# Optimization experiments

Hardware: AMD Instinct MI355X
Metric: run time of the kernel (lower is better)

Reference implementation:

```python
import jax, jax.numpy as jnp
import numpy as np

M, K, V, A = 50, 50, 200, 64  # memory_size, key_dim, value_dim, attention_dim
B, S = 512, 1024


def setup_inputs() -> dict:
    key = jax.random.key(0)
    ks = jax.random.split(key, 12)
    kaiming = lambda k, shape, fan_in: jax.random.normal(k, shape, jnp.float32) * np.sqrt(2.0 / fan_in)
    return {
        "query_embeddings": jax.random.normal(ks[0], (B, S, K), jnp.float32),
        "attention_features": jax.random.normal(ks[1], (B, S, A), jnp.float32),
        "value_memory": jax.random.normal(ks[2], (B, M, V), jnp.float32),
        "key_memory": kaiming(ks[3], (M, K), K),
        "Wc": kaiming(ks[4], (K, K), K),   # correlation_projection
        "bc": jnp.zeros((K,), jnp.float32),
        "Wr": kaiming(ks[5], (A, V), V),   # guided_read_projection
        "br": jnp.zeros((A,), jnp.float32),
        "We": kaiming(ks[6], (V, 2 * A), 2 * A),  # erase_gate
        "be": jnp.zeros((V,), jnp.float32),
        "Wa": kaiming(ks[7], (V, 2 * A), 2 * A),  # add_gate
        "ba": jnp.zeros((V,), jnp.float32),
    }


def reference(query_embeddings, attention_features, value_memory,
              key_memory, Wc, bc, Wr, br, We, be, Wa, ba):
    # update_memory=True path: sequential DKVMN read/erase/add over time.

    def read(mem, q_t, a_t):
        ck = jnp.tanh(q_t @ Wc.T + bc)                     # [B,K]
        w = jax.nn.softmax(ck @ key_memory.T, axis=-1)     # [B,M]
        rc = jnp.einsum('bm,bmv->bv', w, mem) @ Wr.T + br  # [B,A]
        return w, rc

    def write(mem, w, a_t, rc):
        wi = jnp.concatenate([a_t, rc], axis=-1)           # [B,2A]
        erase = jax.nn.sigmoid(wi @ We.T + be)             # [B,V]
        add = jnp.tanh(wi @ Wa.T + ba)                     # [B,V]
        w3 = w[:, :, None]
        return mem * (1.0 - w3 * erase[:, None, :]) + w3 * add[:, None, :]

    def step(mem, xs):
        q_t, a_t = xs
        w, rc = read(mem, q_t, a_t)
        return write(mem, w, a_t, rc), (rc, w)

    # first S-1 steps update memory; last step reads only
    q_seq = jnp.swapaxes(query_embeddings[:, :-1], 0, 1)   # [S-1,B,K]
    a_seq = jnp.swapaxes(attention_features[:, :-1], 0, 1)
    mem_final, (rcs, ws) = jax.lax.scan(step, value_memory, (q_seq, a_seq))
    w_last, rc_last = read(mem_final, query_embeddings[:, -1], attention_features[:, -1])

    read_content = jnp.concatenate([jnp.swapaxes(rcs, 0, 1), rc_last[:, None]], axis=1)  # [B,S,A]
    memory_weights = jnp.concatenate([jnp.swapaxes(ws, 0, 1), w_last[:, None]], axis=1)  # [B,S,M]
    return read_content, mem_final, memory_weights
```

## Files before the change

### kernel.cpp

```cpp
#include <hip/hip_runtime.h>
#include <stdint.h>

#define Md 50
#define Kd 50
#define Vd 200
#define Ad 64
#define Bd 512
#define Sd 1024

__device__ __forceinline__ float fast_tanh(float x) {
    float e = __expf(2.f * x);
    return 1.f - 2.f / (e + 1.f);
}

__device__ __forceinline__ float sigmoidf_(float x) {
    return 1.f / (1.f + __expf(-x));
}

__global__ __launch_bounds__(256)
void wpre_kernel(const float* __restrict__ q_in,
                 const float* __restrict__ key_in,
                 const float* __restrict__ Wc_in,
                 const float* __restrict__ bc_in,
                 float* __restrict__ w_out)
{
    __shared__ float sWc[Kd * 51];
    __shared__ float sKey[Md * 51];
    __shared__ float sbc[Kd];
    __shared__ __align__(16) float sbuf[4][64];

    const int tid = threadIdx.x;
    for (int idx = tid; idx < Kd * Kd; idx += 256) {
        int i = idx / Kd, j = idx % Kd;
        sWc[i * 51 + j]  = Wc_in[idx];
        sKey[i * 51 + j] = key_in[idx];
    }
    if (tid < Kd) sbc[tid] = bc_in[tid];
    __syncthreads();

    const int wv = tid >> 6, ln = tid & 63;
    const int gw = blockIdx.x * 4 + wv;

    for (int r = 0; r < 64; ++r) {
        const size_t row = (size_t)gw * 64 + r;
        float qv = 0.f;
        if (ln < Kd) qv = q_in[row * Kd + ln];
        sbuf[wv][ln] = qv;
        __syncthreads();

        float ck = 0.f;
        if (ln < Kd) {
            const float4* qp = (const float4*)sbuf[wv];
            float acc = sbc[ln];
            #pragma unroll
            for (int c = 0; c < 12; ++c) {
                float4 x = qp[c];
                acc = fmaf(x.x, sWc[ln * 51 + 4 * c + 0], acc);
                acc = fmaf(x.y, sWc[ln * 51 + 4 * c + 1], acc);
                acc = fmaf(x.z, sWc[ln * 51 + 4 * c + 2], acc);
                acc = fmaf(x.w, sWc[ln * 51 + 4 * c + 3], acc);
            }
            float2 x2 = *(const float2*)&sbuf[wv][48];
            acc = fmaf(x2.x, sWc[ln * 51 + 48], acc);
            acc = fmaf(x2.y, sWc[ln * 51 + 49], acc);
            ck = fast_tanh(acc);
        }
        __syncthreads();
        sbuf[wv][ln] = ck;
        __syncthreads();

        float lg = -1e30f;
        if (ln < Md) {
            const float4* cp = (const float4*)sbuf[wv];
            float acc = 0.f;
            #pragma unroll
            for (int c = 0; c < 12; ++c) {
                float4 x = cp[c];
                acc = fmaf(x.x, sKey[ln * 51 + 4 * c + 0], acc);
                acc = fmaf(x.y, sKey[ln * 51 + 4 * c + 1], acc);
                acc = fmaf(x.z, sKey[ln * 51 + 4 * c + 2], acc);
                acc = fmaf(x.w, sKey[ln * 51 + 4 * c + 3], acc);
            }
            float2 x2 = *(const float2*)&sbuf[wv][48];
            acc = fmaf(x2.x, sKey[ln * 51 + 48], acc);
            acc = fmaf(x2.y, sKey[ln * 51 + 49], acc);
            lg = acc;
        }
        float mx = lg;
        #pragma unroll
        for (int off = 32; off > 0; off >>= 1)
            mx = fmaxf(mx, __shfl_xor(mx, off));
        float e = (ln < Md) ? __expf(lg - mx) : 0.f;
        float sm = e;
        #pragma unroll
        for (int off = 32; off > 0; off >>= 1)
            sm += __shfl_xor(sm, off);
        if (ln < Md) w_out[row * Md + ln] = e / sm;
        __syncthreads();
    }
}

__global__ __launch_bounds__(512, 2)
void agm_kernel(const float* __restrict__ a_in,
                const float* __restrict__ mem_in,
                const float* __restrict__ Wr_in,
                const float* __restrict__ br_in,
                const float* __restrict__ We_in,
                const float* __restrict__ be_in,
                const float* __restrict__ Wa_in,
                const float* __restrict__ ba_in,
                const float* __restrict__ w_in,
                float* __restrict__ rc_out,
                float* __restrict__ mem_out)
{
    __shared__ float sWrT[Vd * 66];
    __shared__ float sbr[Ad];
    __shared__ __align__(16) float swi[2][128];
    __shared__ __align__(16) float sw[2][2][64];
    __shared__ float spe[2][2][Vd];
    __shared__ float spa[2][2][Vd];
    __shared__ __align__(8) float srcvI[Vd * 2];

    const int tid = threadIdx.x;
    const int blk = blockIdx.x;
    const int hb  = tid >> 8;
    const int mv  = tid & 255;
    const int bidx = blk * 2 + hb;

    for (int idx = tid; idx < Ad * Vd; idx += 512) {
        int a = idx / Vd, v = idx % Vd;
        sWrT[v * 66 + a] = Wr_in[idx];
    }
    if (tid < Ad) sbr[tid] = br_in[tid];

    const bool isW = (tid < 400);
    const int r5  = tid % 200;
    const int wh5 = tid / 200;
    float WeC[64], WaC[64];
    if (isW) {
        const float4* wep = (const float4*)(We_in + (size_t)r5 * 128 + wh5 * 64);
        const float4* wap = (const float4*)(Wa_in + (size_t)r5 * 128 + wh5 * 64);
        #pragma unroll
        for (int c = 0; c < 16; ++c) {
            float4 ue = wep[c], ua = wap[c];
            WeC[4*c+0]=ue.x; WeC[4*c+1]=ue.y; WeC[4*c+2]=ue.z; WeC[4*c+3]=ue.w;
            WaC[4*c+0]=ua.x; WaC[4*c+1]=ua.y; WaC[4*c+2]=ua.z; WaC[4*c+3]=ua.w;
        }
    } else {
        #pragma unroll
        for (int j = 0; j < 64; ++j) { WeC[j] = 0.f; WaC[j] = 0.f; }
    }

    const bool isM = (mv < Vd);
    float memcol[Md];
    float ebias = 0.f, abias = 0.f;
    if (isM) {
        #pragma unroll
        for (int m = 0; m < Md; ++m)
            memcol[m] = mem_in[(size_t)bidx * Md * Vd + m * Vd + mv];
        ebias = be_in[mv];
        abias = ba_in[mv];
    } else {
        #pragma unroll
        for (int m = 0; m < Md; ++m) memcol[m] = 0.f;
    }

    const int g4 = (tid >> 3) & 31;
    const int c4 = tid & 7;

    const bool isA = (tid < 128);
    const int ahb = tid >> 6, aj = tid & 63;
    const bool isWw = (tid >= 128 && tid < 228);
    const int whb = (tid - 128) / 50, wm = (tid - 128) % 50;

    auto s4_phase = [&](int tt) {
        float q00 = 0.f, q01 = 0.f, q10 = 0.f, q11 = 0.f;
        #pragma unroll
        for (int j = 0; j < 25; ++j) {
            int v = c4 * 25 + j;
            float2 sv = *(const float2*)&srcvI[v * 2];
            float2 wr = *(const float2*)&sWrT[v * 66 + 2 * g4];
            q00 = fmaf(sv.x, wr.x, q00);
            q01 = fmaf(sv.y, wr.x, q01);
            q10 = fmaf(sv.x, wr.y, q10);
            q11 = fmaf(sv.y, wr.y, q11);
        }
        #pragma unroll
        for (int off = 1; off < 8; off <<= 1) {
            q00 += __shfl_xor(q00, off);
            q01 += __shfl_xor(q01, off);
            q10 += __shfl_xor(q10, off);
            q11 += __shfl_xor(q11, off);
        }
        if (c4 == 0) {
            int a0 = 2 * g4, a1 = a0 + 1;
            float rc00 = q00 + sbr[a0], rc01 = q01 + sbr[a0];
            float rc10 = q10 + sbr[a1], rc11 = q11 + sbr[a1];
            swi[0][64 + a0] = rc00; swi[1][64 + a0] = rc01;
            swi[0][64 + a1] = rc10; swi[1][64 + a1] = rc11;
            size_t o0 = ((size_t)(blk * 2 + 0) * Sd + tt) * Ad;
            size_t o1 = ((size_t)(blk * 2 + 1) * Sd + tt) * Ad;
            rc_out[o0 + a0] = rc00; rc_out[o1 + a0] = rc01;
            rc_out[o0 + a1] = rc10; rc_out[o1 + a1] = rc11;
        }
    };

    if (tid < 100) {
        int b = tid / 50, m = tid % 50;
        sw[0][b][m] = w_in[((size_t)(blk * 2 + b) * Sd + 0) * Md + m];
        sw[1][b][m] = w_in[((size_t)(blk * 2 + b) * Sd + 1) * Md + m];
    }
    if (isA) swi[ahb][aj] = a_in[((size_t)(blk * 2 + ahb) * Sd + 0) * Ad + aj];
    float areg = 0.f, wreg = 0.f;
    if (isA) areg = a_in[((size_t)(blk * 2 + ahb) * Sd + 1) * Ad + aj];
    if (isWw) wreg = w_in[((size_t)(blk * 2 + whb) * Sd + 2) * Md + wm];
    __syncthreads();

    if (isM) {
        const float4* w0p = (const float4*)sw[0][hb];
        float rv0 = 0.f, rv1 = 0.f;
        #pragma unroll
        for (int c = 0; c < 12; ++c) {
            float4 wa = w0p[c];
            rv0 = fmaf(wa.x, memcol[4*c+0], rv0);
            rv1 = fmaf(wa.y, memcol[4*c+1], rv1);
            rv0 = fmaf(wa.z, memcol[4*c+2], rv0);
            rv1 = fmaf(wa.w, memcol[4*c+3], rv1);
        }
        float2 wa2 = *(const float2*)&sw[0][hb][48];
        rv0 = fmaf(wa2.x, memcol[48], rv0);
        rv1 = fmaf(wa2.y, memcol[49], rv1);
        srcvI[mv * 2 + hb] = rv0 + rv1;
    }
    __syncthreads();
    if (tid >= 256) s4_phase(0);
    __syncthreads();

    for (int t = 0; t < Sd - 1; ++t) {
        if (isW) {
            const float4* x0p = (const float4*)&swi[0][wh5 * 64];
            const float4* x1p = (const float4*)&swi[1][wh5 * 64];
            float pe0 = 0.f, pa0 = 0.f, pe1 = 0.f, pa1 = 0.f;
            #pragma unroll
            for (int c = 0; c < 16; ++c) {
                float4 x0 = x0p[c];
                float4 x1 = x1p[c];
                float w0 = WeC[4*c+0], w1 = WeC[4*c+1], w2 = WeC[4*c+2], w3 = WeC[4*c+3];
                float u0 = WaC[4*c+0], u1 = WaC[4*c+1], u2 = WaC[4*c+2], u3 = WaC[4*c+3];
                pe0 = fmaf(x0.x, w0, pe0); pe0 = fmaf(x0.y, w1, pe0);
                pe0 = fmaf(x0.z, w2, pe0); pe0 = fmaf(x0.w, w3, pe0);
                pa0 = fmaf(x0.x, u0, pa0); pa0 = fmaf(x0.y, u1, pa0);
                pa0 = fmaf(x0.z, u2, pa0); pa0 = fmaf(x0.w, u3, pa0);
                pe1 = fmaf(x1.x, w0, pe1); pe1 = fmaf(x1.y, w1, pe1);
                pe1 = fmaf(x1.z, w2, pe1); pe1 = fmaf(x1.w, w3, pe1);
                pa1 = fmaf(x1.x, u0, pa1); pa1 = fmaf(x1.y, u1, pa1);
                pa1 = fmaf(x1.z, u2, pa1); pa1 = fmaf(x1.w, u3, pa1);
            }
            spe[wh5][0][r5] = pe0; spe[wh5][1][r5] = pe1;
            spa[wh5][0][r5] = pa0; spa[wh5][1][r5] = pa1;
        }
        __syncthreads();

        if (isM) {
            float se_ = spe[0][hb][mv] + spe[1][hb][mv] + ebias;
            float sa_ = spa[0][hb][mv] + spa[1][hb][mv] + abias;
            float ev = sigmoidf_(se_);
            float av = fast_tanh(sa_);
            const float4* w0p = (const float4*)sw[t & 1][hb];
            const float4* w1p = (const float4*)sw[(t + 1) & 1][hb];
            float rv0 = 0.f, rv1 = 0.f;
            #pragma unroll
            for (int c = 0; c < 12; ++c) {
                float4 wa = w0p[c];
                float4 wb = w1p[c];
                { float mc = memcol[4*c+0]; mc = fmaf(wa.x, fmaf(-ev, mc, av), mc);
                  memcol[4*c+0] = mc; rv0 = fmaf(wb.x, mc, rv0); }
                { float mc = memcol[4*c+1]; mc = fmaf(wa.y, fmaf(-ev, mc, av), mc);
                  memcol[4*c+1] = mc; rv1 = fmaf(wb.y, mc, rv1); }
                { float mc = memcol[4*c+2]; mc = fmaf(wa.z, fmaf(-ev, mc, av), mc);
                  memcol[4*c+2] = mc; rv0 = fmaf(wb.z, mc, rv0); }
                { float mc = memcol[4*c+3]; mc = fmaf(wa.w, fmaf(-ev, mc, av), mc);
                  memcol[4*c+3] = mc; rv1 = fmaf(wb.w, mc, rv1); }
            }
            {
                float2 wa2 = *(const float2*)&sw[t & 1][hb][48];
                float2 wb2 = *(const float2*)&sw[(t + 1) & 1][hb][48];
                { float mc = memcol[48]; mc = fmaf(wa2.x, fmaf(-ev, mc, av), mc);
                  memcol[48] = mc; rv0 = fmaf(wb2.x, mc, rv0); }
                { float mc = memcol[49]; mc = fmaf(wa2.y, fmaf(-ev, mc, av), mc);
                  memcol[49] = mc; rv1 = fmaf(wb2.y, mc, rv1); }
            }
            srcvI[mv * 2 + hb] = rv0 + rv1;
        }
        __syncthreads();

        if (tid >= 256) {
            s4_phase(t + 1);
        } else {
            if (isA) swi[ahb][aj] = areg;
            if (isWw && t + 2 < Sd) sw[t & 1][whb][wm] = wreg;
        }
        if (isA && t + 2 < Sd)
            areg = a_in[((size_t)(blk * 2 + ahb) * Sd + (t + 2)) * Ad + aj];
        if (isWw && t + 3 < Sd)
            wreg = w_in[((size_t)(blk * 2 + whb) * Sd + (t + 3)) * Md + wm];
        __syncthreads();
    }

    if (isM) {
        #pragma unroll
        for (int m = 0; m < Md; ++m)
            mem_out[(size_t)bidx * Md * Vd + m * Vd + mv] = memcol[m];
    }
}

extern "C" void kernel_launch(void* const* d_in, const int* in_sizes, int n_in,
                              void* d_out, int out_size, void* d_ws, size_t ws_size,
                              hipStream_t stream) {
    const float* q   = (const float*)d_in[0];
    const float* a   = (const float*)d_in[1];
    const float* mem = (const float*)d_in[2];
    const float* key = (const float*)d_in[3];
    const float* Wc  = (const float*)d_in[4];
    const float* bc  = (const float*)d_in[5];
    const float* Wr  = (const float*)d_in[6];
    const float* br  = (const float*)d_in[7];
    const float* We  = (const float*)d_in[8];
    const float* be  = (const float*)d_in[9];
    const float* Wa  = (const float*)d_in[10];
    const float* ba  = (const float*)d_in[11];

    float* out = (float*)d_out;
    float* rc_out  = out;
    float* mem_out = rc_out + (size_t)Bd * Sd * Ad;
    float* w_out   = mem_out + (size_t)Bd * Md * Vd;

    hipLaunchKernelGGL(wpre_kernel, dim3(2048), dim3(256), 0, stream,
                       q, key, Wc, bc, w_out);
    hipLaunchKernelGGL(agm_kernel, dim3(256), dim3(512), 0, stream,
                       a, mem, Wr, br, We, be, Wa, ba, w_out,
                       rc_out, mem_out);
}
```

Measured before the change: 5.746 ms.

## Redistribute recurrent DKVMN work across 1024 threads with register-resident weights

```diff
diff --git a/kernel.cpp b/kernel.cpp
--- a/kernel.cpp
+++ b/kernel.cpp
@@ -100,7 +100,7 @@
     }
 }
 
-__global__ __launch_bounds__(512, 2)
+__global__ __launch_bounds__(1024)
 void agm_kernel(const float* __restrict__ a_in,
                 const float* __restrict__ mem_in,
                 const float* __restrict__ Wr_in,
@@ -113,204 +113,269 @@
                 float* __restrict__ rc_out,
                 float* __restrict__ mem_out)
 {
-    __shared__ float sWrT[Vd * 66];
+    __shared__ __align__(16) float swi[2][128];
+    __shared__ __align__(16) float sw_[2][2][2][28];
+    __shared__ __align__(16) float srcvP2[4][224];
+    __shared__ __align__(16) float eradI2[4][256];
+    __shared__ __align__(16) float spr[16][2][64];
     __shared__ float sbr[Ad];
-    __shared__ __align__(16) float swi[2][128];
-    __shared__ __align__(16) float sw[2][2][64];
-    __shared__ float spe[2][2][Vd];
-    __shared__ float spa[2][2][Vd];
-    __shared__ __align__(8) float srcvI[Vd * 2];
+    __shared__ float sbe[Vd];
+    __shared__ float sba[Vd];
 
     const int tid = threadIdx.x;
     const int blk = blockIdx.x;
-    const int hb  = tid >> 8;
-    const int mv  = tid & 255;
-    const int bidx = blk * 2 + hb;
-
-    for (int idx = tid; idx < Ad * Vd; idx += 512) {
-        int a = idx / Vd, v = idx % Vd;
-        sWrT[v * 66 + a] = Wr_in[idx];
-    }
-    if (tid < Ad) sbr[tid] = br_in[tid];
-
-    const bool isW = (tid < 400);
-    const int r5  = tid % 200;
-    const int wh5 = tid / 200;
-    float WeC[64], WaC[64];
-    if (isW) {
-        const float4* wep = (const float4*)(We_in + (size_t)r5 * 128 + wh5 * 64);
-        const float4* wap = (const float4*)(Wa_in + (size_t)r5 * 128 + wh5 * 64);
-        #pragma unroll
-        for (int c = 0; c < 16; ++c) {
-            float4 ue = wep[c], ua = wap[c];
-            WeC[4*c+0]=ue.x; WeC[4*c+1]=ue.y; WeC[4*c+2]=ue.z; WeC[4*c+3]=ue.w;
-            WaC[4*c+0]=ua.x; WaC[4*c+1]=ua.y; WaC[4*c+2]=ua.z; WaC[4*c+3]=ua.w;
+    const int wv  = tid >> 6;
+    const int ln  = tid & 63;
+
+    const int r1 = tid >> 2, q1 = tid & 3;
+    const int p2mh = wv >> 3, p2bt = (wv >> 2) & 1;
+    const int p2v  = ((wv & 3) << 6) | ln;
+    const int p2b  = blk * 2 + p2bt;
+    const int c3 = wv & 7, h3 = wv >> 3;
+
+    float WC[64];
+    if (r1 < Vd) {
+        const float4* wep = (const float4*)(We_in + (size_t)r1 * 128 + q1 * 32);
+        const float4* wap = (const float4*)(Wa_in + (size_t)r1 * 128 + q1 * 32);
+        #pragma unroll
+        for (int c = 0; c < 8; ++c) {
+            float4 u = wep[c];
+            WC[4*c+0] = u.x; WC[4*c+1] = u.y; WC[4*c+2] = u.z; WC[4*c+3] = u.w;
+        }
+        #pragma unroll
+        for (int c = 0; c < 8; ++c) {
+            float4 u = wap[c];
+            WC[32+4*c+0] = u.x; WC[32+4*c+1] = u.y; WC[32+4*c+2] = u.z; WC[32+4*c+3] = u.w;
         }
     } else {
         #pragma unroll
-        for (int j = 0; j < 64; ++j) { WeC[j] = 0.f; WaC[j] = 0.f; }
-    }
-
-    const bool isM = (mv < Vd);
-    float memcol[Md];
-    float ebias = 0.f, abias = 0.f;
-    if (isM) {
-        #pragma unroll
-        for (int m = 0; m < Md; ++m)
-            memcol[m] = mem_in[(size_t)bidx * Md * Vd + m * Vd + mv];
-        ebias = be_in[mv];
-        abias = ba_in[mv];
+        for (int j = 0; j < 64; ++j) WC[j] = 0.f;
+    }
+
+    float WrS[13];
+    {
+        const int nj = h3 ? 12 : 13;
+        const int vb = c3 * 25 + h3 * 13;
+        #pragma unroll
+        for (int j = 0; j < 13; ++j)
+            WrS[j] = (j < nj) ? Wr_in[(size_t)ln * Vd + vb + j] : 0.f;
+    }
+
+    float memcol[25];
+    if (p2v < Vd) {
+        #pragma unroll
+        for (int j = 0; j < 25; ++j)
+            memcol[j] = mem_in[(size_t)p2b * Md * Vd + (p2mh * 25 + j) * Vd + p2v];
     } else {
         #pragma unroll
-        for (int m = 0; m < Md; ++m) memcol[m] = 0.f;
-    }
-
-    const int g4 = (tid >> 3) & 31;
-    const int c4 = tid & 7;
-
-    const bool isA = (tid < 128);
-    const int ahb = tid >> 6, aj = tid & 63;
-    const bool isWw = (tid >= 128 && tid < 228);
-    const int whb = (tid - 128) / 50, wm = (tid - 128) % 50;
-
-    auto s4_phase = [&](int tt) {
-        float q00 = 0.f, q01 = 0.f, q10 = 0.f, q11 = 0.f;
-        #pragma unroll
-        for (int j = 0; j < 25; ++j) {
-            int v = c4 * 25 + j;
-            float2 sv = *(const float2*)&srcvI[v * 2];
-            float2 wr = *(const float2*)&sWrT[v * 66 + 2 * g4];
-            q00 = fmaf(sv.x, wr.x, q00);
-            q01 = fmaf(sv.y, wr.x, q01);
-            q10 = fmaf(sv.x, wr.y, q10);
-            q11 = fmaf(sv.y, wr.y, q11);
-        }
-        #pragma unroll
-        for (int off = 1; off < 8; off <<= 1) {
-            q00 += __shfl_xor(q00, off);
-            q01 += __shfl_xor(q01, off);
-            q10 += __shfl_xor(q10, off);
-            q11 += __shfl_xor(q11, off);
-        }
-        if (c4 == 0) {
-            int a0 = 2 * g4, a1 = a0 + 1;
-            float rc00 = q00 + sbr[a0], rc01 = q01 + sbr[a0];
-            float rc10 = q10 + sbr[a1], rc11 = q11 + sbr[a1];
-            swi[0][64 + a0] = rc00; swi[1][64 + a0] = rc01;
-            swi[0][64 + a1] = rc10; swi[1][64 + a1] = rc11;
-            size_t o0 = ((size_t)(blk * 2 + 0) * Sd + tt) * Ad;
-            size_t o1 = ((size_t)(blk * 2 + 1) * Sd + tt) * Ad;
-            rc_out[o0 + a0] = rc00; rc_out[o1 + a0] = rc01;
-            rc_out[o0 + a1] = rc10; rc_out[o1 + a1] = rc11;
-        }
-    };
-
-    if (tid < 100) {
-        int b = tid / 50, m = tid % 50;
-        sw[0][b][m] = w_in[((size_t)(blk * 2 + b) * Sd + 0) * Md + m];
-        sw[1][b][m] = w_in[((size_t)(blk * 2 + b) * Sd + 1) * Md + m];
-    }
-    if (isA) swi[ahb][aj] = a_in[((size_t)(blk * 2 + ahb) * Sd + 0) * Ad + aj];
-    float areg = 0.f, wreg = 0.f;
-    if (isA) areg = a_in[((size_t)(blk * 2 + ahb) * Sd + 1) * Ad + aj];
-    if (isWw) wreg = w_in[((size_t)(blk * 2 + whb) * Sd + 2) * Md + wm];
+        for (int j = 0; j < 25; ++j) memcol[j] = 0.f;
+    }
+    const int p2off = (p2v / 25) * 28 + (p2v % 25);
+    const int p2pl  = p2mh * 2 + p2bt;
+
+    const bool isAld = (tid >= 896);
+    const int  abt = wv & 1;
+    const float* aload = a_in + (size_t)(blk * 2 + abt) * Sd * Ad + ln;
+    const bool isWld = (tid >= 256 && tid < 356);
+    const int  wub = isWld ? (tid - 256) : 0;
+    const int  wbt = wub / 50;
+    const int  wm  = wub - wbt * 50;
+    const float* wload = w_in + (size_t)(blk * 2 + wbt) * Sd * Md + wm;
+    float* wcom = &sw_[0][wbt][wm / 25][wm % 25];
+
+    if (tid < 200) {
+        int s = tid / 100, rst = tid % 100;
+        int bt = rst / 50, m = rst % 50;
+        sw_[s][bt][m / 25][m % 25] = w_in[((size_t)(blk * 2 + bt) * Sd + s) * Md + m];
+    } else if (tid < 328) {
+        int u = tid - 200;
+        swi[u >> 6][u & 63] = a_in[(size_t)(blk * 2 + (u >> 6)) * Sd * Ad + (u & 63)];
+    } else if (tid < 392) {
+        sbr[tid - 328] = br_in[tid - 328];
+    } else if (tid < 592) {
+        sbe[tid - 392] = be_in[tid - 392];
+    } else if (tid < 792) {
+        sba[tid - 592] = ba_in[tid - 592];
+    }
+    float areg = 0.f, anext = 0.f, wreg = 0.f, wnext = 0.f, rcval = 0.f;
+    if (isAld) areg = aload[(size_t)1 * Ad];
     __syncthreads();
 
-    if (isM) {
-        const float4* w0p = (const float4*)sw[0][hb];
-        float rv0 = 0.f, rv1 = 0.f;
-        #pragma unroll
-        for (int c = 0; c < 12; ++c) {
-            float4 wa = w0p[c];
-            rv0 = fmaf(wa.x, memcol[4*c+0], rv0);
-            rv1 = fmaf(wa.y, memcol[4*c+1], rv1);
-            rv0 = fmaf(wa.z, memcol[4*c+2], rv0);
-            rv1 = fmaf(wa.w, memcol[4*c+3], rv1);
-        }
-        float2 wa2 = *(const float2*)&sw[0][hb][48];
-        rv0 = fmaf(wa2.x, memcol[48], rv0);
-        rv1 = fmaf(wa2.y, memcol[49], rv1);
-        srcvI[mv * 2 + hb] = rv0 + rv1;
+    if (p2v < Vd) {
+        const float4* wp = (const float4*)&sw_[0][p2bt][p2mh][0];
+        float rv = 0.f;
+        #pragma unroll
+        for (int c = 0; c < 6; ++c) {
+            float4 w4 = wp[c];
+            rv = fmaf(w4.x, memcol[4*c+0], rv);
+            rv = fmaf(w4.y, memcol[4*c+1], rv);
+            rv = fmaf(w4.z, memcol[4*c+2], rv);
+            rv = fmaf(w4.w, memcol[4*c+3], rv);
+        }
+        rv = fmaf(sw_[0][p2bt][p2mh][24], memcol[24], rv);
+        srcvP2[p2pl][p2off] = rv;
     }
     __syncthreads();
-    if (tid >= 256) s4_phase(0);
-    __syncthreads();
-
-    for (int t = 0; t < Sd - 1; ++t) {
-        if (isW) {
-            const float4* x0p = (const float4*)&swi[0][wh5 * 64];
-            const float4* x1p = (const float4*)&swi[1][wh5 * 64];
-            float pe0 = 0.f, pa0 = 0.f, pe1 = 0.f, pa1 = 0.f;
-            #pragma unroll
-            for (int c = 0; c < 16; ++c) {
-                float4 x0 = x0p[c];
-                float4 x1 = x1p[c];
-                float w0 = WeC[4*c+0], w1 = WeC[4*c+1], w2 = WeC[4*c+2], w3 = WeC[4*c+3];
-                float u0 = WaC[4*c+0], u1 = WaC[4*c+1], u2 = WaC[4*c+2], u3 = WaC[4*c+3];
-                pe0 = fmaf(x0.x, w0, pe0); pe0 = fmaf(x0.y, w1, pe0);
-                pe0 = fmaf(x0.z, w2, pe0); pe0 = fmaf(x0.w, w3, pe0);
-                pa0 = fmaf(x0.x, u0, pa0); pa0 = fmaf(x0.y, u1, pa0);
-                pa0 = fmaf(x0.z, u2, pa0); pa0 = fmaf(x0.w, u3, pa0);
-                pe1 = fmaf(x1.x, w0, pe1); pe1 = fmaf(x1.y, w1, pe1);
-                pe1 = fmaf(x1.z, w2, pe1); pe1 = fmaf(x1.w, w3, pe1);
-                pa1 = fmaf(x1.x, u0, pa1); pa1 = fmaf(x1.y, u1, pa1);
-                pa1 = fmaf(x1.z, u2, pa1); pa1 = fmaf(x1.w, u3, pa1);
-            }
-            spe[wh5][0][r5] = pe0; spe[wh5][1][r5] = pe1;
-            spa[wh5][0][r5] = pa0; spa[wh5][1][r5] = pa1;
-        }
-        __syncthreads();
-
-        if (isM) {
-            float se_ = spe[0][hb][mv] + spe[1][hb][mv] + ebias;
-            float sa_ = spa[0][hb][mv] + spa[1][hb][mv] + abias;
-            float ev = sigmoidf_(se_);
-            float av = fast_tanh(sa_);
-            const float4* w0p = (const float4*)sw[t & 1][hb];
-            const float4* w1p = (const float4*)sw[(t + 1) & 1][hb];
-            float rv0 = 0.f, rv1 = 0.f;
-            #pragma unroll
-            for (int c = 0; c < 12; ++c) {
+
+    for (int t = 0; t < Sd; ++t) {
+        {
+            const int cb = c3 * 28 + h3 * 12;
+            const float* b00 = &srcvP2[0][cb];
+            const float* b01 = &srcvP2[1][cb];
+            const float* b10 = &srcvP2[2][cb];
+            const float* b11 = &srcvP2[3][cb];
+            float a0 = 0.f, a1 = 0.f;
+            if (h3 == 0) {
+                #pragma unroll
+                for (int c = 0; c < 3; ++c) {
+                    float4 u0 = *(const float4*)(b00 + 4*c);
+                    float4 u2 = *(const float4*)(b10 + 4*c);
+                    float4 u1 = *(const float4*)(b01 + 4*c);
+                    float4 u3 = *(const float4*)(b11 + 4*c);
+                    a0 = fmaf(u0.x + u2.x, WrS[4*c+0], a0);
+                    a0 = fmaf(u0.y + u2.y, WrS[4*c+1], a0);
+                    a0 = fmaf(u0.z + u2.z, WrS[4*c+2], a0);
+                    a0 = fmaf(u0.w + u2.w, WrS[4*c+3], a0);
+                    a1 = fmaf(u1.x + u3.x, WrS[4*c+0], a1);
+                    a1 = fmaf(u1.y + u3.y, WrS[4*c+1], a1);
+                    a1 = fmaf(u1.z + u3.z, WrS[4*c+2], a1);
+                    a1 = fmaf(u1.w + u3.w, WrS[4*c+3], a1);
+                }
+                a0 = fmaf(b00[12] + b10[12], WrS[12], a0);
+                a1 = fmaf(b01[12] + b11[12], WrS[12], a1);
+            } else {
+                float4 u0 = *(const float4*)(b00);
+                float4 u2 = *(const float4*)(b10);
+                float4 u1 = *(const float4*)(b01);
+                float4 u3 = *(const float4*)(b11);
+                a0 = fmaf(u0.y + u2.y, WrS[0], a0);
+                a0 = fmaf(u0.z + u2.z, WrS[1], a0);
+                a0 = fmaf(u0.w + u2.w, WrS[2], a0);
+                a1 = fmaf(u1.y + u3.y, WrS[0], a1);
+                a1 = fmaf(u1.z + u3.z, WrS[1], a1);
+                a1 = fmaf(u1.w + u3.w, WrS[2], a1);
+                #pragma unroll
+                for (int c = 0; c < 2; ++c) {
+                    u0 = *(const float4*)(b00 + 4 + 4*c);
+                    u2 = *(const float4*)(b10 + 4 + 4*c);
+                    u1 = *(const float4*)(b01 + 4 + 4*c);
+                    u3 = *(const float4*)(b11 + 4 + 4*c);
+                    a0 = fmaf(u0.x + u2.x, WrS[3+4*c+0], a0);
+                    a0 = fmaf(u0.y + u2.y, WrS[3+4*c+1], a0);
+                    a0 = fmaf(u0.z + u2.z, WrS[3+4*c+2], a0);
+                    a0 = fmaf(u0.w + u2.w, WrS[3+4*c+3], a0);
+                    a1 = fmaf(u1.x + u3.x, WrS[3+4*c+0], a1);
+                    a1 = fmaf(u1.y + u3.y, WrS[3+4*c+1], a1);
+                    a1 = fmaf(u1.z + u3.z, WrS[3+4*c+2], a1);
+                    a1 = fmaf(u1.w + u3.w, WrS[3+4*c+3], a1);
+                }
+                u0 = *(const float4*)(b00 + 12);
+                u2 = *(const float4*)(b10 + 12);
+                u1 = *(const float4*)(b01 + 12);
+                u3 = *(const float4*)(b11 + 12);
+                a0 = fmaf(u0.x + u2.x, WrS[11], a0);
+                a1 = fmaf(u1.x + u3.x, WrS[11], a1);
+            }
+            spr[wv][0][ln] = a0;
+            spr[wv][1][ln] = a1;
+        }
+        __syncthreads();
+
+        if (tid < 128) {
+            const int ra = tid & 63, rbt = tid >> 6;
+            float s = sbr[ra];
+            #pragma unroll
+            for (int w = 0; w < 16; ++w) s += spr[w][rbt][ra];
+            swi[rbt][64 + ra] = s;
+            rcval = s;
+        }
+        if (isWld && t >= 1 && t < Sd - 1)
+            wcom[((t + 1) & 1) * 112] = wreg;
+        __syncthreads();
+
+        if (t == Sd - 1) break;
+
+        if (tid < 128)
+            rc_out[((size_t)(blk * 2 + (tid >> 6)) * Sd + t) * Ad + (tid & 63)] = rcval;
+        if (isWld && t + 2 < Sd) wnext = wload[(size_t)(t + 2) * Md];
+        if (isAld && t + 2 < Sd) anext = aload[(size_t)(t + 2) * Ad];
+        if (r1 < Vd) {
+            float pe0 = 0.f, po0 = 0.f, pe1 = 0.f, po1 = 0.f;
+            const float4* xap = (const float4*)&swi[0][q1 * 32];
+            const float4* xbp = (const float4*)&swi[1][q1 * 32];
+            #pragma unroll
+            for (int c = 0; c < 8; ++c) {
+                float4 x = xap[c];
+                pe0 = fmaf(x.x, WC[4*c+0], pe0);
+                pe0 = fmaf(x.y, WC[4*c+1], pe0);
+                pe0 = fmaf(x.z, WC[4*c+2], pe0);
+                pe0 = fmaf(x.w, WC[4*c+3], pe0);
+                po0 = fmaf(x.x, WC[32+4*c+0], po0);
+                po0 = fmaf(x.y, WC[32+4*c+1], po0);
+                po0 = fmaf(x.z, WC[32+4*c+2], po0);
+                po0 = fmaf(x.w, WC[32+4*c+3], po0);
+            }
+            #pragma unroll
+            for (int c = 0; c < 8; ++c) {
+                float4 x = xbp[c];
+                pe1 = fmaf(x.x, WC[4*c+0], pe1);
+                pe1 = fmaf(x.y, WC[4*c+1], pe1);
+                pe1 = fmaf(x.z, WC[4*c+2], pe1);
+                pe1 = fmaf(x.w, WC[4*c+3], pe1);
+                po1 = fmaf(x.x, WC[32+4*c+0], po1);
+                po1 = fmaf(x.y, WC[32+4*c+1], po1);
+                po1 = fmaf(x.z, WC[32+4*c+2], po1);
+                po1 = fmaf(x.w, WC[32+4*c+3], po1);
+            }
+            pe0 += __shfl_xor(pe0, 1); pe0 += __shfl_xor(pe0, 2);
+            po0 += __shfl_xor(po0, 1); po0 += __shfl_xor(po0, 2);
+            pe1 += __shfl_xor(pe1, 1); pe1 += __shfl_xor(pe1, 2);
+            po1 += __shfl_xor(po1, 1); po1 += __shfl_xor(po1, 2);
+            const float pre = (q1 & 2) ? pe1 : pe0;
+            const float pod = (q1 & 2) ? po1 : po0;
+            const float lin = (q1 & 1) ? (pod + sba[r1]) : (pre + sbe[r1]);
+            const float sg  = sigmoidf_((q1 & 1) ? (lin + lin) : lin);
+            eradI2[q1][r1] = (q1 & 1) ? fmaf(2.f, sg, -1.f) : sg;
+        }
+        __syncthreads();
+
+        if (p2v < Vd) {
+            const float ev = eradI2[2 * p2bt][p2v];
+            const float av = eradI2[2 * p2bt + 1][p2v];
+            const float4* w0p = (const float4*)&sw_[t & 1][p2bt][p2mh][0];
+            const float4* w1p = (const float4*)&sw_[(t + 1) & 1][p2bt][p2mh][0];
+            float rv = 0.f;
+            #pragma unroll
+            for (int c = 0; c < 6; ++c) {
                 float4 wa = w0p[c];
                 float4 wb = w1p[c];
-                { float mc = memcol[4*c+0]; mc = fmaf(wa.x, fmaf(-ev, mc, av), mc);
-                  memcol[4*c+0] = mc; rv0 = fmaf(wb.x, mc, rv0); }
-                { float mc = memcol[4*c+1]; mc = fmaf(wa.y, fmaf(-ev, mc, av), mc);
-                  memcol[4*c+1] = mc; rv1 = fmaf(wb.y, mc, rv1); }
-                { float mc = memcol[4*c+2]; mc = fmaf(wa.z, fmaf(-ev, mc, av), mc);
-                  memcol[4*c+2] = mc; rv0 = fmaf(wb.z, mc, rv0); }
-                { float mc = memcol[4*c+3]; mc = fmaf(wa.w, fmaf(-ev, mc, av), mc);
-                  memcol[4*c+3] = mc; rv1 = fmaf(wb.w, mc, rv1); }
+                { float mc = memcol[4*c+0]; mc = fmaf(wa.x, fmaf(-ev, mc, av), mc); memcol[4*c+0] = mc; rv = fmaf(wb.x, mc, rv); }
+                { float mc = memcol[4*c+1]; mc = fmaf(wa.y, fmaf(-ev, mc, av), mc); memcol[4*c+1] = mc; rv = fmaf(wb.y, mc, rv); }
+                { float mc = memcol[4*c+2]; mc = fmaf(wa.z, fmaf(-ev, mc, av), mc); memcol[4*c+2] = mc; rv = fmaf(wb.z, mc, rv); }
+                { float mc = memcol[4*c+3]; mc = fmaf(wa.w, fmaf(-ev, mc, av), mc); memcol[4*c+3] = mc; rv = fmaf(wb.w, mc, rv); }
             }
             {
-                float2 wa2 = *(const float2*)&sw[t & 1][hb][48];
-                float2 wb2 = *(const float2*)&sw[(t + 1) & 1][hb][48];
-                { float mc = memcol[48]; mc = fmaf(wa2.x, fmaf(-ev, mc, av), mc);
-                  memcol[48] = mc; rv0 = fmaf(wb2.x, mc, rv0); }
-                { float mc = memcol[49]; mc = fmaf(wa2.y, fmaf(-ev, mc, av), mc);
-                  memcol[49] = mc; rv1 = fmaf(wb2.y, mc, rv1); }
-            }
-            srcvI[mv * 2 + hb] = rv0 + rv1;
-        }
-        __syncthreads();
-
-        if (tid >= 256) {
-            s4_phase(t + 1);
-        } else {
-            if (isA) swi[ahb][aj] = areg;
-            if (isWw && t + 2 < Sd) sw[t & 1][whb][wm] = wreg;
-        }
-        if (isA && t + 2 < Sd)
-            areg = a_in[((size_t)(blk * 2 + ahb) * Sd + (t + 2)) * Ad + aj];
-        if (isWw && t + 3 < Sd)
-            wreg = w_in[((size_t)(blk * 2 + whb) * Sd + (t + 3)) * Md + wm];
-        __syncthreads();
-    }
-
-    if (isM) {
-        #pragma unroll
-        for (int m = 0; m < Md; ++m)
-            mem_out[(size_t)bidx * Md * Vd + m * Vd + mv] = memcol[m];
+                float wa = ((const float*)w0p)[24];
+                float wb = ((const float*)w1p)[24];
+                float mc = memcol[24]; mc = fmaf(wa, fmaf(-ev, mc, av), mc); memcol[24] = mc; rv = fmaf(wb, mc, rv);
+            }
+            srcvP2[p2pl][p2off] = rv;
+        }
+        if (isAld) {
+            swi[abt][ln] = areg;
+            areg = anext;
+        }
+        if (isWld) wreg = wnext;
+        __syncthreads();
+    }
+
+    if (tid < 128)
+        rc_out[((size_t)(blk * 2 + (tid >> 6)) * Sd + (Sd - 1)) * Ad + (tid & 63)] = rcval;
+
+    if (p2v < Vd) {
+        #pragma unroll
+        for (int j = 0; j < 25; ++j)
+            mem_out[(size_t)p2b * Md * Vd + (p2mh * 25 + j) * Vd + p2v] = memcol[j];
     }
 }
 
@@ -337,7 +402,7 @@
 
     hipLaunchKernelGGL(wpre_kernel, dim3(2048), dim3(256), 0, stream,
                        q, key, Wc, bc, w_out);
-    hipLaunchKernelGGL(agm_kernel, dim3(256), dim3(512), 0, stream,
+    hipLaunchKernelGGL(agm_kernel, dim3(256), dim3(1024), 0, stream,
                        a, mem, Wr, br, We, be, Wa, ba, w_out,
                        rc_out, mem_out);
 }
```

Result: slower. 18.18 ms (+216.5%).
